# Optimization experiments

Measured on AMD Instinct MI355X. Metric: run time of the kernel, lower is better.

Reference implementation:

```python
import jax, jax.numpy as jnp
import numpy as np

B, D_IN, H, A, L, HEADS, C = 1024, 512, 768, 5001, 4, 2, 2
N_DATA = 56000.0
NEG = -1e30


def _gru_step(x, h, Wih, Whh, bih, bhh):
    # torch nn.GRU gate order: r, z, n
    gi = x @ Wih + bih            # [B, 3H]
    gh = h @ Whh + bhh            # [B, 3H]
    i_r, i_z, i_n = jnp.split(gi, 3, axis=-1)
    h_r, h_z, h_n = jnp.split(gh, 3, axis=-1)
    r = jax.nn.sigmoid(i_r + h_r)
    z = jax.nn.sigmoid(i_z + h_z)
    n = jnp.tanh(i_n + r * h_n)
    return (1.0 - z) * n + z * h


def _atom_selector(cls, mask, Wih, Whh, bih, bhh, hW, hb, ae_w, key):
    # cls: [B, H]; mask: [B, A] int32 (mutable copy); dropout in eval mode (identity)
    h = jnp.zeros_like(cls)
    cur_in = cls
    ae_const = jax.lax.stop_gradient(ae_w)
    probs = []
    max_index = None
    rows = jnp.arange(B)
    for j in range(L):
        h = _gru_step(cur_in, h, Wih, Whh, bih, bhh)
        logits = h @ hW + hb                      # [B, A]
        if j == 0:
            col0 = jnp.where(mask.sum(axis=-1) == 0, 1, mask[:, 0])
            mask = mask.at[:, 0].set(col0)
        else:
            mask = jnp.where((max_index == 0)[:, None], 0, mask)
            mask = mask.at[:, 0].set(1)
        masked = jnp.where(mask > 0, logits, NEG)
        u = jax.random.uniform(jax.random.fold_in(key, j), (B, A), minval=1e-9, maxval=1.0)
        g = -jnp.log(-jnp.log(u))
        y_soft = jax.nn.softmax(masked + g, axis=-1)  # tau = 1
        ind = jnp.argmax(y_soft, axis=-1)             # [B]
        y_hard = jax.nn.one_hot(ind, A, dtype=y_soft.dtype)
        prob = y_hard + y_soft - jax.lax.stop_gradient(y_soft)  # straight-through
        mask = mask.at[rows, ind].set(0)              # scatter-zero chosen atoms
        probs.append(prob)
        max_index = ind
        cur_in = cls + prob @ ae_const                # atom embedding feedback
    return jnp.stack(probs, axis=1)                   # [B, L, A]


def reference(x, x_mask, W1, b1, W2, b2, W3, b3, gru_Wih, gru_Whh, gru_bih, gru_bhh,
              head_W, head_b, ae_w, ce_Wmu, ce_bmu, ce_Wcov, ce_bcov, alpha):
    # linear_base MLP
    h = jax.nn.relu(x @ W1 + b1)
    h = jax.nn.relu(h @ W2 + b2)
    h = h @ W3 + b3                                   # cls embedding [B, H]
    key = jax.random.key(42)
    atom_probs, cps = [], []
    for i in range(HEADS):
        ap = _atom_selector(h, x_mask, gru_Wih[i], gru_Whh[i], gru_bih[i], gru_bhh[i],
                            head_W[i], head_b[i], ae_w, jax.random.fold_in(key, i))
        atom_probs.append(ap)
        # consequent estimator stand-in: mu [B,C], coverage [B]
        pooled = ap.mean(axis=1)                      # [B, A]
        mu = jax.nn.sigmoid(pooled @ ce_Wmu + ce_bmu)
        coverage = jax.nn.sigmoid(pooled @ ce_Wcov + ce_bcov)
        n = coverage * N_DATA
        sf = (alpha[0] / n)[:, None]                  # [B, 1] -> broadcast to [B, C]
        cp = (mu + sf) / (1.0 + 2.0 * sf)
        cps.append(cp)
    mat_cp = jnp.stack(cps, axis=1)                   # [B, HEADS, C]
    out = jnp.log(mat_cp.mean(axis=1))                # [B, C]
    return out, jnp.stack(atom_probs, axis=1), mat_cp


def setup_inputs() -> dict:
    key = jax.random.key(0)
    ks = jax.random.split(key, 16)
    s = 0.02
    nrm = lambda k, sh: jax.random.normal(k, sh, dtype=jnp.float32) * s
    return {
        'x': jax.random.normal(ks[0], (B, D_IN), dtype=jnp.float32),
        'x_mask': jax.random.randint(ks[1], (B, A), 0, 2, dtype=jnp.int32),
        'W1': nrm(ks[2], (D_IN, H)), 'b1': jnp.zeros((H,), jnp.float32),
        'W2': nrm(ks[3], (H, H)), 'b2': jnp.zeros((H,), jnp.float32),
        'W3': nrm(ks[4], (H, H)), 'b3': jnp.zeros((H,), jnp.float32),
        'gru_Wih': nrm(ks[5], (HEADS, H, 3 * H)), 'gru_Whh': nrm(ks[6], (HEADS, H, 3 * H)),
        'gru_bih': jnp.zeros((HEADS, 3 * H), jnp.float32), 'gru_bhh': jnp.zeros((HEADS, 3 * H), jnp.float32),
        'head_W': nrm(ks[7], (HEADS, H, A)), 'head_b': jnp.zeros((HEADS, A), jnp.float32),
        'ae_w': nrm(ks[8], (A, H)),
        'ce_Wmu': nrm(ks[9], (A, C)), 'ce_bmu': jnp.zeros((C,), jnp.float32),
        'ce_Wcov': nrm(ks[10], (A,)), 'ce_bcov': jnp.zeros((), jnp.float32),
        'alpha': jnp.ones((1,), jnp.float32),
    }
```

## Files before the change

kernel.cpp:

```cpp
#include <hip/hip_runtime.h>
#include <hip/hip_bf16.h>
#include <stdint.h>
#include <stddef.h>

#define B_DIM   1024
#define DIN     512
#define H_DIM   768
#define A_DIM   5001
#define NHEADS  2
#define NSTEPS  4
#define C_DIM   2
#define NEG_VAL -1e30f
#define BH      (B_DIM * H_DIM)

typedef unsigned short u16;
typedef __attribute__((ext_vector_type(8))) short v8s;
typedef __attribute__((ext_vector_type(4))) float v4f;

typedef const __attribute__((address_space(1))) uint32_t* gas_ptr;
typedef __attribute__((address_space(3))) uint32_t* las_ptr;

__device__ __forceinline__ void load_lds16(const void* g, void* l) {
  __builtin_amdgcn_global_load_lds((gas_ptr)g, (las_ptr)l, 16, 0, 0);
}

__host__ __device__ inline uint32_t rotl32(uint32_t x, int d) {
  return (x << d) | (x >> (32 - d));
}

__host__ __device__ inline void threefry2x32(uint32_t k0, uint32_t k1,
                                             uint32_t x0, uint32_t x1,
                                             uint32_t& o0, uint32_t& o1) {
  uint32_t ks2 = k0 ^ k1 ^ 0x1BD11BDAu;
  x0 += k0; x1 += k1;
#define TFR(d) { x0 += x1; x1 = rotl32(x1, (d)); x1 ^= x0; }
  TFR(13) TFR(15) TFR(26) TFR(6)  x0 += k1;  x1 += ks2 + 1u;
  TFR(17) TFR(29) TFR(16) TFR(24) x0 += ks2; x1 += k0 + 2u;
  TFR(13) TFR(15) TFR(26) TFR(6)  x0 += k0;  x1 += k1 + 3u;
  TFR(17) TFR(29) TFR(16) TFR(24) x0 += k1;  x1 += ks2 + 4u;
  TFR(13) TFR(15) TFR(26) TFR(6)  x0 += ks2; x1 += k0 + 5u;
#undef TFR
  o0 = x0; o1 = x1;
}

__device__ inline float gumbel_noise(uint32_t k0, uint32_t k1, uint32_t idx) {
  uint32_t o0, o1;
  threefry2x32(k0, k1, 0u, idx, o0, o1);
  uint32_t bits = o0 ^ o1;
  float f = __uint_as_float(0x3f800000u | (bits >> 9)) - 1.0f;
  float u = fmaxf(1e-9f, f * (1.0f - 1e-9f) + 1e-9f);
  return -logf(-logf(u));
}

__device__ inline float sigmoidf_(float x) { return 0.5f * tanhf(0.5f * x) + 0.5f; }

__device__ inline void split_bf16(float x, u16& hi, u16& lo) {
  __hip_bfloat16 h = __float2bfloat16(x);
  float hf = __bfloat162float(h);
  __hip_bfloat16 l = __float2bfloat16(x - hf);
  hi = *(const u16*)&h;
  lo = *(const u16*)&l;
}

__global__ __launch_bounds__(256) void split_kernel(
    const float* __restrict__ in, u16* __restrict__ hi, u16* __restrict__ lo, int n) {
  int idx = blockIdx.x * blockDim.x + threadIdx.x;
  if (idx >= n) return;
  u16 h, l;
  split_bf16(in[idx], h, l);
  hi[idx] = h; lo[idx] = l;
}

struct TS { const float* W; u16* hi; u16* lo; int K; int N; };
struct TS9 { TS t[9]; };

__global__ __launch_bounds__(256) void transpose_split_b(TS9 ts) {
  const TS p = ts.t[blockIdx.z];
  const int k0 = blockIdx.y * 32, n0 = blockIdx.x * 32;
  if (k0 >= p.K || n0 >= p.N) return;
  __shared__ float tile[32][33];
  const int tx = threadIdx.x & 31, ty = threadIdx.x >> 5;
#pragma unroll
  for (int r = ty; r < 32; r += 8) {
    int n = n0 + tx;
    tile[r][tx] = (n < p.N) ? p.W[(size_t)(k0 + r) * p.N + n] : 0.0f;
  }
  __syncthreads();
#pragma unroll
  for (int r = ty; r < 32; r += 8) {
    int n = n0 + r, k = k0 + tx;
    if (n < p.N) {
      u16 h, l;
      split_bf16(tile[tx][r], h, l);
      p.hi[(size_t)n * p.K + k] = h;
      p.lo[(size_t)n * p.K + k] = l;
    }
  }
}

struct GemmS {
  const u16* Ah[4]; const u16* Al[4];
  const u16* Bh[4]; const u16* Bl[4];
  const float* bias[4];
  float* C[4];
  u16* Ch[4]; u16* Cl[4];
  int N[4]; int nbx[4]; long long ldc[4]; int act[4]; int dup[4];
};

__global__ __launch_bounds__(256, 2) void gemm_mfma(GemmS gs, int K, int nby) {
  const int e = blockIdx.y;
  const int nwg = gridDim.x;
  const int chunk = nwg >> 3;
  const int lid = (blockIdx.x & 7) * chunk + (blockIdx.x >> 3);
  const int by = lid % nby;
  const int bx = lid / nby;
  if (bx >= gs.nbx[e]) return;
  const int bm = by * 128, bn = bx * 128;
  const int N = gs.N[e];

  __shared__ __align__(16) u16 lds[2][4][128 * 32];

  const int tid = threadIdx.x;
  const int wv = tid >> 6, ln = tid & 63;
  const int wr = wv >> 1, wc = wv & 1;
  const int lk = ln >> 4;
  const int lm = ln & 15;
  const int fswz = (lm >> 1) & 3;

  const int lrow = ln >> 2;
  const int slot = (ln & 3) ^ ((lrow >> 1) & 3);
  const u16* tsrc = (wv == 0) ? gs.Ah[e] : (wv == 1) ? gs.Al[e]
                  : (wv == 2) ? gs.Bh[e] : gs.Bl[e];
  const int isB = (wv >= 2);
  const int rowbase = isB ? bn : bm;

#define STAGE(B, K0)                                                  \
  {                                                                   \
    _Pragma("unroll")                                                 \
    for (int i = 0; i < 8; ++i) {                                     \
      int gr = rowbase + i * 16 + lrow;                               \
      if (isB && gr >= N) gr = N - 1;                                 \
      load_lds16(tsrc + (size_t)gr * K + (K0) + slot * 8,             \
                 (void*)&lds[B][wv][i * 512]);                        \
    }                                                                 \
  }

  v4f acc[4][4];
#pragma unroll
  for (int i = 0; i < 4; ++i)
#pragma unroll
    for (int j = 0; j < 4; ++j) acc[i][j] = (v4f){0.f, 0.f, 0.f, 0.f};

  STAGE(0, 0)
  int buf = 0;
  for (int k0 = 0; k0 < K; k0 += 32) {
    __syncthreads();
    if (k0 + 32 < K) STAGE(buf ^ 1, k0 + 32)

    const u16* LAh = lds[buf][0];
    const u16* LAl = lds[buf][1];
    const u16* LBh = lds[buf][2];
    const u16* LBl = lds[buf][3];
    v8s ah[4], al[4], bh[4], bl[4];
#pragma unroll
    for (int mi = 0; mi < 4; ++mi) {
      const int r = wr * 64 + mi * 16 + lm;
      const int off = r * 32 + ((lk ^ fswz) * 8);
      ah[mi] = *(const v8s*)&LAh[off];
      al[mi] = *(const v8s*)&LAl[off];
    }
#pragma unroll
    for (int ni = 0; ni < 4; ++ni) {
      const int r = wc * 64 + ni * 16 + lm;
      const int off = r * 32 + ((lk ^ fswz) * 8);
      bh[ni] = *(const v8s*)&LBh[off];
      bl[ni] = *(const v8s*)&LBl[off];
    }
#pragma unroll
    for (int mi = 0; mi < 4; ++mi)
#pragma unroll
      for (int ni = 0; ni < 4; ++ni)
        acc[mi][ni] = __builtin_amdgcn_mfma_f32_16x16x32_bf16(ah[mi], bh[ni], acc[mi][ni], 0, 0, 0);
#pragma unroll
    for (int mi = 0; mi < 4; ++mi)
#pragma unroll
      for (int ni = 0; ni < 4; ++ni)
        acc[mi][ni] = __builtin_amdgcn_mfma_f32_16x16x32_bf16(ah[mi], bl[ni], acc[mi][ni], 0, 0, 0);
#pragma unroll
    for (int mi = 0; mi < 4; ++mi)
#pragma unroll
      for (int ni = 0; ni < 4; ++ni)
        acc[mi][ni] = __builtin_amdgcn_mfma_f32_16x16x32_bf16(al[mi], bh[ni], acc[mi][ni], 0, 0, 0);

    buf ^= 1;
  }

  const float* bias = gs.bias[e];
  const long long ldc = gs.ldc[e];
  const int act = gs.act[e];
  float* Cf = gs.C[e];
  u16* ch = gs.Ch[e]; u16* cl = gs.Cl[e];
  const int dup = gs.dup[e];
#pragma unroll
  for (int mi = 0; mi < 4; ++mi) {
    const int m = bm + wr * 64 + mi * 16 + lk * 4;
#pragma unroll
    for (int ni = 0; ni < 4; ++ni) {
      const int n = bn + wc * 64 + ni * 16 + lm;
      if (n < N) {
        const float bv = bias[n];
#pragma unroll
        for (int r = 0; r < 4; ++r) {
          float v = acc[mi][ni][r] + bv;
          if (act) v = fmaxf(v, 0.0f);
          const size_t ix = (size_t)(m + r) * ldc + n;
          if (Cf) Cf[ix] = v;
          if (ch) {
            u16 hh, ll;
            split_bf16(v, hh, ll);
            ch[ix] = hh; cl[ix] = ll;
            if (dup) { ch[ix + (size_t)BH] = hh; cl[ix + (size_t)BH] = ll; }
          }
        }
      }
    }
  }
#undef STAGE
}

__global__ __launch_bounds__(256) void gru_combine_first(
    const float* __restrict__ gi2, const float* __restrict__ gbhh, float* __restrict__ h2,
    u16* __restrict__ h_hi, u16* __restrict__ h_lo) {
  int idx = blockIdx.x * blockDim.x + threadIdx.x;
  if (idx >= 2 * BH) return;
  int e = idx / BH, rem = idx % BH;
  int b = rem / H_DIM, c = rem - b * H_DIM;
  const float* gib = gi2 + ((size_t)e * B_DIM + b) * 3 * H_DIM;
  const float* bb = gbhh + (size_t)e * 3 * H_DIM;
  float ir = gib[c], iz = gib[H_DIM + c], inn = gib[2 * H_DIM + c];
  float hr = bb[c], hz = bb[H_DIM + c], hn = bb[2 * H_DIM + c];
  float r = sigmoidf_(ir + hr);
  float z = sigmoidf_(iz + hz);
  float n = tanhf(inn + r * hn);
  float hv = (1.0f - z) * n + z * 0.0f;
  h2[idx] = hv;
  u16 h, l;
  split_bf16(hv, h, l);
  h_hi[idx] = h; h_lo[idx] = l;
}

__global__ __launch_bounds__(256) void gru_combine_kernel(
    const float* __restrict__ gi2, const float* __restrict__ gh2, float* __restrict__ h2,
    u16* __restrict__ h_hi, u16* __restrict__ h_lo) {
  int idx = blockIdx.x * blockDim.x + threadIdx.x;
  if (idx >= 2 * BH) return;
  int e = idx / BH, rem = idx % BH;
  int b = rem / H_DIM, c = rem - b * H_DIM;
  const float* gib = gi2 + ((size_t)e * B_DIM + b) * 3 * H_DIM;
  const float* ghb = gh2 + ((size_t)e * B_DIM + b) * 3 * H_DIM;
  float ir = gib[c], iz = gib[H_DIM + c], inn = gib[2 * H_DIM + c];
  float hr = ghb[c], hz = ghb[H_DIM + c], hn = ghb[2 * H_DIM + c];
  float r = sigmoidf_(ir + hr);
  float z = sigmoidf_(iz + hz);
  float n = tanhf(inn + r * hn);
  float hv = (1.0f - z) * n + z * h2[idx];
  h2[idx] = hv;
  u16 h, l;
  split_bf16(hv, h, l);
  h_hi[idx] = h; h_lo[idx] = l;
}

#define STH 256
#define PER_TH 20

__global__ __launch_bounds__(STH) void sample_kernel(
    float* __restrict__ probs, const int* __restrict__ x_mask,
    int* __restrict__ indb, int j, uint4 keys,
    const float* __restrict__ cls, const float* __restrict__ ae_w,
    u16* __restrict__ cur_hi, u16* __restrict__ cur_lo, int docur) {
  int b = blockIdx.x;
  int e = blockIdx.y;
  int t = threadIdx.x;
  uint32_t k0 = (e == 0) ? keys.x : keys.z;
  uint32_t k1 = (e == 0) ? keys.y : keys.w;
  __shared__ float rv[STH];
  __shared__ int ri[STH];
  __shared__ int s_ind;

  float* prow = probs + (((size_t)b * NHEADS + e) * NSTEPS + j) * A_DIM;
  const int* mrow = x_mask + (size_t)b * A_DIM;

  int prev[3];
  bool dead = false;
  for (int tt = 0; tt < j; ++tt) {
    prev[tt] = indb[(e * NSTEPS + tt) * B_DIM + b];
    if (prev[tt] == 0) dead = true;
  }

  bool rowany = true;
  if (j == 0) {
    int any = 0;
    for (int a = t; a < A_DIM; a += STH) any |= mrow[a];
    ri[t] = any; __syncthreads();
    for (int s = STH / 2; s > 0; s >>= 1) {
      if (t < s) ri[t] |= ri[t + s];
      __syncthreads();
    }
    rowany = (ri[0] != 0);
    __syncthreads();
  }

  float v[PER_TH];
  float lmax = -3.0e38f;
#pragma unroll
  for (int s = 0; s < PER_TH; ++s) {
    int a = t + s * STH;
    float val = -3.0e38f;
    if (a < A_DIM) {
      int m;
      if (j == 0) {
        m = (a == 0) ? (rowany ? mrow[0] : 1) : mrow[a];
      } else if (a == 0) {
        m = 1;
      } else if (dead) {
        m = 0;
      } else {
        m = mrow[a];
        if (m) {
          for (int tt = 0; tt < j; ++tt)
            if (prev[tt] == a) { m = 0; break; }
        }
      }
      if (m > 0)
        val = prow[a] + gumbel_noise(k0, k1, (uint32_t)(b * A_DIM + a));
    }
    v[s] = val;
    lmax = fmaxf(lmax, val);
  }

  rv[t] = lmax; __syncthreads();
  for (int s = STH / 2; s > 0; s >>= 1) {
    if (t < s) rv[t] = fmaxf(rv[t], rv[t + s]);
    __syncthreads();
  }
  float m = rv[0]; __syncthreads();

  float lsum = 0.0f;
#pragma unroll
  for (int s = 0; s < PER_TH; ++s) {
    int a = t + s * STH;
    float ev = (a < A_DIM && v[s] > -1.0e37f) ? expf(v[s] - m) : 0.0f;
    v[s] = ev; lsum += ev;
  }
  rv[t] = lsum; __syncthreads();
  for (int s = STH / 2; s > 0; s >>= 1) {
    if (t < s) rv[t] += rv[t + s];
    __syncthreads();
  }
  float ssum = rv[0]; __syncthreads();

  float besty = -1.0f; int besti = A_DIM;
#pragma unroll
  for (int s = 0; s < PER_TH; ++s) {
    int a = t + s * STH;
    if (a < A_DIM) {
      float y = v[s] / ssum;
      if (y > besty) { besty = y; besti = a; }
    }
  }
  rv[t] = besty; ri[t] = besti; __syncthreads();
  for (int s = STH / 2; s > 0; s >>= 1) {
    if (t < s) {
      float y2 = rv[t + s]; int i2 = ri[t + s];
      if (y2 > rv[t] || (y2 == rv[t] && i2 < ri[t])) { rv[t] = y2; ri[t] = i2; }
    }
    __syncthreads();
  }
  if (t == 0) { s_ind = ri[0]; indb[(e * NSTEPS + j) * B_DIM + b] = ri[0]; }
  __syncthreads();
  int ind = s_ind;

  for (int a = t; a < A_DIM; a += STH) prow[a] = (a == ind) ? 1.0f : 0.0f;

  if (docur) {
    const float* crow = cls + (size_t)b * H_DIM;
    const float* arow = ae_w + (size_t)ind * H_DIM;
    u16* chh = cur_hi + (size_t)e * BH + (size_t)b * H_DIM;
    u16* cll = cur_lo + (size_t)e * BH + (size_t)b * H_DIM;
    for (int c = t; c < H_DIM; c += STH) {
      float vv = crow[c] + arow[c];
      u16 hh, ll;
      split_bf16(vv, hh, ll);
      chh[c] = hh; cll[c] = ll;
    }
  }
}

__global__ __launch_bounds__(256) void head_final_kernel(
    const int* __restrict__ indb, const float* __restrict__ Wmu,
    const float* __restrict__ bmu, const float* __restrict__ Wcov,
    const float* __restrict__ bcov, const float* __restrict__ alpha,
    float* __restrict__ matcp) {
  int idx = blockIdx.x * blockDim.x + threadIdx.x;
  if (idx >= NHEADS * B_DIM) return;
  int e = idx / B_DIM, b = idx - e * B_DIM;
  float a0 = 0.0f, a1 = 0.0f, ac = 0.0f;
  for (int j = 0; j < NSTEPS; ++j) {
    int ind = indb[(e * NSTEPS + j) * B_DIM + b];
    a0 += 0.25f * Wmu[(size_t)ind * C_DIM + 0];
    a1 += 0.25f * Wmu[(size_t)ind * C_DIM + 1];
    ac += 0.25f * Wcov[ind];
  }
  float mu0 = sigmoidf_(a0 + bmu[0]);
  float mu1 = sigmoidf_(a1 + bmu[1]);
  float cov = sigmoidf_(ac + bcov[0]);
  float n = cov * 56000.0f;
  float sf = alpha[0] / n;
  float denom = 1.0f + 2.0f * sf;
  matcp[((size_t)b * NHEADS + e) * C_DIM + 0] = (mu0 + sf) / denom;
  matcp[((size_t)b * NHEADS + e) * C_DIM + 1] = (mu1 + sf) / denom;
}

__global__ __launch_bounds__(256) void final_out_kernel(
    const float* __restrict__ matcp, float* __restrict__ out) {
  int idx = blockIdx.x * blockDim.x + threadIdx.x;
  if (idx >= B_DIM * C_DIM) return;
  int b = idx / C_DIM, c = idx - b * C_DIM;
  float s = matcp[((size_t)b * NHEADS + 0) * C_DIM + c] +
            matcp[((size_t)b * NHEADS + 1) * C_DIM + c];
  out[idx] = logf(s * 0.5f);
}

extern "C" void kernel_launch(void* const* d_in, const int* in_sizes, int n_in,
                              void* d_out, int out_size, void* d_ws, size_t ws_size,
                              hipStream_t stream) {
  const float* x     = (const float*)d_in[0];
  const int*   xmask = (const int*)d_in[1];
  const float* W1 = (const float*)d_in[2];  const float* b1 = (const float*)d_in[3];
  const float* W2 = (const float*)d_in[4];  const float* b2 = (const float*)d_in[5];
  const float* W3 = (const float*)d_in[6];  const float* b3 = (const float*)d_in[7];
  const float* gWih = (const float*)d_in[8];  const float* gWhh = (const float*)d_in[9];
  const float* gbih = (const float*)d_in[10]; const float* gbhh = (const float*)d_in[11];
  const float* hW = (const float*)d_in[12];   const float* hb = (const float*)d_in[13];
  const float* ae_w = (const float*)d_in[14];
  const float* Wmu  = (const float*)d_in[15]; const float* bmu  = (const float*)d_in[16];
  const float* Wcov = (const float*)d_in[17]; const float* bcov = (const float*)d_in[18];
  const float* alpha = (const float*)d_in[19];

  float* out = (float*)d_out;
  float* probs = out + (size_t)B_DIM * C_DIM;
  float* matcp = probs + (size_t)B_DIM * NHEADS * NSTEPS * A_DIM;

  const int HG = 3 * H_DIM;
  uint8_t* wsp = (uint8_t*)d_ws;
  auto alloc = [&](size_t bytes) {
    uint8_t* p = wsp;
    wsp += (bytes + 255) & ~(size_t)255;
    return p;
  };
  float* cls  = (float*)alloc((size_t)BH * 4);
  float* h2   = (float*)alloc((size_t)2 * BH * 4);
  float* gi2  = (float*)alloc((size_t)2 * B_DIM * HG * 4);
  float* gh2  = (float*)alloc((size_t)2 * B_DIM * HG * 4);
  u16* h_hi   = (u16*)alloc((size_t)2 * BH * 2);
  u16* h_lo   = (u16*)alloc((size_t)2 * BH * 2);
  u16* cur_hi = (u16*)alloc((size_t)2 * BH * 2);
  u16* cur_lo = (u16*)alloc((size_t)2 * BH * 2);
  u16* WihT_h = (u16*)alloc((size_t)2 * HG * H_DIM * 2);
  u16* WihT_l = (u16*)alloc((size_t)2 * HG * H_DIM * 2);
  u16* WhhT_h = (u16*)alloc((size_t)2 * HG * H_DIM * 2);
  u16* WhhT_l = (u16*)alloc((size_t)2 * HG * H_DIM * 2);
  u16* hWT_h  = (u16*)alloc((size_t)2 * A_DIM * H_DIM * 2);
  u16* hWT_l  = (u16*)alloc((size_t)2 * A_DIM * H_DIM * 2);
  u16* x_hi   = (u16*)alloc((size_t)B_DIM * DIN * 2);
  u16* x_lo   = (u16*)alloc((size_t)B_DIM * DIN * 2);
  u16* t1_hi  = (u16*)alloc((size_t)BH * 2);
  u16* t1_lo  = (u16*)alloc((size_t)BH * 2);
  u16* t2_hi  = (u16*)alloc((size_t)BH * 2);
  u16* t2_lo  = (u16*)alloc((size_t)BH * 2);
  u16* W1T_h  = (u16*)alloc((size_t)H_DIM * DIN * 2);
  u16* W1T_l  = (u16*)alloc((size_t)H_DIM * DIN * 2);
  u16* W2T_h  = (u16*)alloc((size_t)H_DIM * H_DIM * 2);
  u16* W2T_l  = (u16*)alloc((size_t)H_DIM * H_DIM * 2);
  u16* W3T_h  = (u16*)alloc((size_t)H_DIM * H_DIM * 2);
  u16* W3T_l  = (u16*)alloc((size_t)H_DIM * H_DIM * 2);
  int* indb   = (int*)alloc((size_t)NHEADS * NSTEPS * B_DIM * 4);

  dim3 blk(256);

  {
    TS9 ts;
    ts.t[0] = {gWih,                    WihT_h,                    WihT_l,                    H_DIM, HG};
    ts.t[1] = {gWih + (size_t)H_DIM*HG, WihT_h + (size_t)HG*H_DIM, WihT_l + (size_t)HG*H_DIM, H_DIM, HG};
    ts.t[2] = {gWhh,                    WhhT_h,                    WhhT_l,                    H_DIM, HG};
    ts.t[3] = {gWhh + (size_t)H_DIM*HG, WhhT_h + (size_t)HG*H_DIM, WhhT_l + (size_t)HG*H_DIM, H_DIM, HG};
    ts.t[4] = {hW,                          hWT_h,                           hWT_l,                           H_DIM, A_DIM};
    ts.t[5] = {hW + (size_t)H_DIM*A_DIM,    hWT_h + (size_t)A_DIM*H_DIM,     hWT_l + (size_t)A_DIM*H_DIM,     H_DIM, A_DIM};
    ts.t[6] = {W1, W1T_h, W1T_l, DIN,   H_DIM};
    ts.t[7] = {W2, W2T_h, W2T_l, H_DIM, H_DIM};
    ts.t[8] = {W3, W3T_h, W3T_l, H_DIM, H_DIM};
    transpose_split_b<<<dim3((A_DIM + 31) / 32, H_DIM / 32, 9), blk, 0, stream>>>(ts);
  }
  split_kernel<<<(B_DIM * DIN + 255) / 256, blk, 0, stream>>>(x, x_hi, x_lo, B_DIM * DIN);

  auto setE = [](GemmS& g, int e, const u16* ah, const u16* al, const u16* bhp, const u16* blp,
                 const float* bias, float* Cf, u16* chp, u16* clp,
                 int N, int nbx, long long ldc, int act, int dup) {
    g.Ah[e] = ah; g.Al[e] = al; g.Bh[e] = bhp; g.Bl[e] = blp;
    g.bias[e] = bias; g.C[e] = Cf; g.Ch[e] = chp; g.Cl[e] = clp;
    g.N[e] = N; g.nbx[e] = nbx; g.ldc[e] = ldc; g.act[e] = act; g.dup[e] = dup;
  };

  {
    GemmS g{};
    setE(g, 0, x_hi, x_lo, W1T_h, W1T_l, b1, nullptr, t1_hi, t1_lo, H_DIM, H_DIM / 128, H_DIM, 1, 0);
    gemm_mfma<<<dim3((H_DIM / 128) * 8, 1), blk, 0, stream>>>(g, DIN, 8);
  }
  {
    GemmS g{};
    setE(g, 0, t1_hi, t1_lo, W2T_h, W2T_l, b2, nullptr, t2_hi, t2_lo, H_DIM, H_DIM / 128, H_DIM, 1, 0);
    gemm_mfma<<<dim3((H_DIM / 128) * 8, 1), blk, 0, stream>>>(g, H_DIM, 8);
  }
  {
    GemmS g{};
    setE(g, 0, t2_hi, t2_lo, W3T_h, W3T_l, b3, cls, cur_hi, cur_lo, H_DIM, H_DIM / 128, H_DIM, 0, 1);
    gemm_mfma<<<dim3((H_DIM / 128) * 8, 1), blk, 0, stream>>>(g, H_DIM, 8);
  }

  uint32_t bk0 = 0u, bk1 = 42u;
  uint32_t hk[2][2];
  threefry2x32(bk0, bk1, 0u, 0u, hk[0][0], hk[0][1]);
  threefry2x32(bk0, bk1, 0u, 1u, hk[1][0], hk[1][1]);

  const int NBX_L = (A_DIM + 127) / 128;
  const int NBX_G = HG / 128;

  for (int j = 0; j < NSTEPS; ++j) {
    if (j == 0) {
      GemmS g{};
      for (int head = 0; head < NHEADS; ++head)
        setE(g, head, cur_hi + (size_t)head * BH, cur_lo + (size_t)head * BH,
             WihT_h + (size_t)head * HG * H_DIM, WihT_l + (size_t)head * HG * H_DIM,
             gbih + (size_t)head * HG, gi2 + (size_t)head * B_DIM * HG, nullptr, nullptr,
             HG, NBX_G, HG, 0, 0);
      gemm_mfma<<<dim3(NBX_G * 8, 2), blk, 0, stream>>>(g, H_DIM, 8);
      gru_combine_first<<<(2 * BH + 255) / 256, blk, 0, stream>>>(gi2, gbhh, h2, h_hi, h_lo);
    } else {
      GemmS g{};
      for (int head = 0; head < NHEADS; ++head) {
        setE(g, head * 2 + 0, cur_hi + (size_t)head * BH, cur_lo + (size_t)head * BH,
             WihT_h + (size_t)head * HG * H_DIM, WihT_l + (size_t)head * HG * H_DIM,
             gbih + (size_t)head * HG, gi2 + (size_t)head * B_DIM * HG, nullptr, nullptr,
             HG, NBX_G, HG, 0, 0);
        setE(g, head * 2 + 1, h_hi + (size_t)head * BH, h_lo + (size_t)head * BH,
             WhhT_h + (size_t)head * HG * H_DIM, WhhT_l + (size_t)head * HG * H_DIM,
             gbhh + (size_t)head * HG, gh2 + (size_t)head * B_DIM * HG, nullptr, nullptr,
             HG, NBX_G, HG, 0, 0);
      }
      gemm_mfma<<<dim3(NBX_G * 8, 4), blk, 0, stream>>>(g, H_DIM, 8);
      gru_combine_kernel<<<(2 * BH + 255) / 256, blk, 0, stream>>>(gi2, gh2, h2, h_hi, h_lo);
    }

    {
      GemmS g{};
      for (int head = 0; head < NHEADS; ++head)
        setE(g, head, h_hi + (size_t)head * BH, h_lo + (size_t)head * BH,
             hWT_h + (size_t)head * A_DIM * H_DIM, hWT_l + (size_t)head * A_DIM * H_DIM,
             hb + (size_t)head * A_DIM, probs + (size_t)(head * NSTEPS + j) * A_DIM,
             nullptr, nullptr, A_DIM, NBX_L, (long long)NHEADS * NSTEPS * A_DIM, 0, 0);
      gemm_mfma<<<dim3(NBX_L * 8, 2), blk, 0, stream>>>(g, H_DIM, 8);
    }

    uint32_t s00, s01, s10, s11;
    threefry2x32(hk[0][0], hk[0][1], 0u, (uint32_t)j, s00, s01);
    threefry2x32(hk[1][0], hk[1][1], 0u, (uint32_t)j, s10, s11);
    uint4 keys; keys.x = s00; keys.y = s01; keys.z = s10; keys.w = s11;
    sample_kernel<<<dim3(B_DIM, NHEADS), dim3(STH), 0, stream>>>(
        probs, xmask, indb, j, keys, cls, ae_w, cur_hi, cur_lo, (j < NSTEPS - 1) ? 1 : 0);
  }

  head_final_kernel<<<(NHEADS * B_DIM + 255) / 256, blk, 0, stream>>>(
      indb, Wmu, bmu, Wcov, bcov, alpha, matcp);
  final_out_kernel<<<(B_DIM * C_DIM + 255) / 256, blk, 0, stream>>>(matcp, out);
}
```

Baseline: 865.8 us.

## Shrink GEMM N-tile to 64, drop LDS double buffering, raise occupancy

The MFMA GEMM now uses 128x64 output tiles instead of 128x128, halving the B-operand LDS footprint and accumulator registers, and launch bounds rise to allow four blocks per CU. The double-buffered prefetch pipeline is replaced by a single-buffer load, sync, compute, sync loop. The aim is more concurrent waves and more blocks for the small-N GEMMs, at the cost of less reuse of A tiles and no overlap of global-to-LDS loads with compute within a block. HG becomes a macro, which is a cleanup.

```diff
diff --git a/kernel.cpp b/kernel.cpp
--- a/kernel.cpp
+++ b/kernel.cpp
@@ -12,6 +12,7 @@
 #define C_DIM   2
 #define NEG_VAL -1e30f
 #define BH      (B_DIM * H_DIM)
+#define HG      (3 * H_DIM)
 
 typedef unsigned short u16;
 typedef __attribute__((ext_vector_type(8))) short v8s;
@@ -107,7 +108,7 @@
   int N[4]; int nbx[4]; long long ldc[4]; int act[4]; int dup[4];
 };
 
-__global__ __launch_bounds__(256, 2) void gemm_mfma(GemmS gs, int K, int nby) {
+__global__ __launch_bounds__(256, 4) void gemm_mfma(GemmS gs, int K, int nby) {
   const int e = blockIdx.y;
   const int nwg = gridDim.x;
   const int chunk = nwg >> 3;
@@ -115,10 +116,11 @@
   const int by = lid % nby;
   const int bx = lid / nby;
   if (bx >= gs.nbx[e]) return;
-  const int bm = by * 128, bn = bx * 128;
+  const int bm = by * 128, bn = bx * 64;
   const int N = gs.N[e];
 
-  __shared__ __align__(16) u16 lds[2][4][128 * 32];
+  __shared__ __align__(16) u16 ldsA[2][128 * 32];
+  __shared__ __align__(16) u16 ldsB[2][64 * 32];
 
   const int tid = threadIdx.x;
   const int wv = tid >> 6, ln = tid & 63;
@@ -133,66 +135,56 @@
                   : (wv == 2) ? gs.Bh[e] : gs.Bl[e];
   const int isB = (wv >= 2);
   const int rowbase = isB ? bn : bm;
-
-#define STAGE(B, K0)                                                  \
-  {                                                                   \
-    _Pragma("unroll")                                                 \
-    for (int i = 0; i < 8; ++i) {                                     \
-      int gr = rowbase + i * 16 + lrow;                               \
-      if (isB && gr >= N) gr = N - 1;                                 \
-      load_lds16(tsrc + (size_t)gr * K + (K0) + slot * 8,             \
-                 (void*)&lds[B][wv][i * 512]);                        \
-    }                                                                 \
-  }
-
-  v4f acc[4][4];
+  u16* ldst = isB ? ldsB[wv - 2] : ldsA[wv];
+  const int nIss = isB ? 4 : 8;
+
+  v4f acc[4][2];
 #pragma unroll
   for (int i = 0; i < 4; ++i)
 #pragma unroll
-    for (int j = 0; j < 4; ++j) acc[i][j] = (v4f){0.f, 0.f, 0.f, 0.f};
-
-  STAGE(0, 0)
-  int buf = 0;
-  for (int k0 = 0; k0 < K; k0 += 32) {
+    for (int j = 0; j < 2; ++j) acc[i][j] = (v4f){0.f, 0.f, 0.f, 0.f};
+
+  for (int kt = 0; kt < K; kt += 32) {
+    for (int i = 0; i < nIss; ++i) {
+      int gr = rowbase + i * 16 + lrow;
+      if (isB && gr >= N) gr = N - 1;
+      const u16* gp = tsrc + (size_t)gr * K + kt + slot * 8;
+      load_lds16(gp, (void*)&ldst[i * 512]);
+    }
     __syncthreads();
-    if (k0 + 32 < K) STAGE(buf ^ 1, k0 + 32)
-
-    const u16* LAh = lds[buf][0];
-    const u16* LAl = lds[buf][1];
-    const u16* LBh = lds[buf][2];
-    const u16* LBl = lds[buf][3];
-    v8s ah[4], al[4], bh[4], bl[4];
+
+    v8s ah[4], al[4], bh[2], bl[2];
 #pragma unroll
     for (int mi = 0; mi < 4; ++mi) {
       const int r = wr * 64 + mi * 16 + lm;
       const int off = r * 32 + ((lk ^ fswz) * 8);
-      ah[mi] = *(const v8s*)&LAh[off];
-      al[mi] = *(const v8s*)&LAl[off];
-    }
-#pragma unroll
-    for (int ni = 0; ni < 4; ++ni) {
-      const int r = wc * 64 + ni * 16 + lm;
+      ah[mi] = *(const v8s*)&ldsA[0][off];
+      al[mi] = *(const v8s*)&ldsA[1][off];
+    }
+#pragma unroll
+    for (int ni = 0; ni < 2; ++ni) {
+      const int r = wc * 32 + ni * 16 + lm;
       const int off = r * 32 + ((lk ^ fswz) * 8);
-      bh[ni] = *(const v8s*)&LBh[off];
-      bl[ni] = *(const v8s*)&LBl[off];
+      bh[ni] = *(const v8s*)&ldsB[0][off];
+      bl[ni] = *(const v8s*)&ldsB[1][off];
     }
 #pragma unroll
     for (int mi = 0; mi < 4; ++mi)
 #pragma unroll
-      for (int ni = 0; ni < 4; ++ni)
+      for (int ni = 0; ni < 2; ++ni)
         acc[mi][ni] = __builtin_amdgcn_mfma_f32_16x16x32_bf16(ah[mi], bh[ni], acc[mi][ni], 0, 0, 0);
 #pragma unroll
     for (int mi = 0; mi < 4; ++mi)
 #pragma unroll
-      for (int ni = 0; ni < 4; ++ni)
+      for (int ni = 0; ni < 2; ++ni)
         acc[mi][ni] = __builtin_amdgcn_mfma_f32_16x16x32_bf16(ah[mi], bl[ni], acc[mi][ni], 0, 0, 0);
 #pragma unroll
     for (int mi = 0; mi < 4; ++mi)
 #pragma unroll
-      for (int ni = 0; ni < 4; ++ni)
+      for (int ni = 0; ni < 2; ++ni)
         acc[mi][ni] = __builtin_amdgcn_mfma_f32_16x16x32_bf16(al[mi], bh[ni], acc[mi][ni], 0, 0, 0);
 
-    buf ^= 1;
+    __syncthreads();
   }
 
   const float* bias = gs.bias[e];
@@ -205,8 +197,8 @@
   for (int mi = 0; mi < 4; ++mi) {
     const int m = bm + wr * 64 + mi * 16 + lk * 4;
 #pragma unroll
-    for (int ni = 0; ni < 4; ++ni) {
-      const int n = bn + wc * 64 + ni * 16 + lm;
+    for (int ni = 0; ni < 2; ++ni) {
+      const int n = bn + wc * 32 + ni * 16 + lm;
       if (n < N) {
         const float bv = bias[n];
 #pragma unroll
@@ -225,7 +217,6 @@
       }
     }
   }
-#undef STAGE
 }
 
 __global__ __launch_bounds__(256) void gru_combine_first(
@@ -235,8 +226,8 @@
   if (idx >= 2 * BH) return;
   int e = idx / BH, rem = idx % BH;
   int b = rem / H_DIM, c = rem - b * H_DIM;
-  const float* gib = gi2 + ((size_t)e * B_DIM + b) * 3 * H_DIM;
-  const float* bb = gbhh + (size_t)e * 3 * H_DIM;
+  const float* gib = gi2 + ((size_t)e * B_DIM + b) * HG;
+  const float* bb = gbhh + (size_t)e * HG;
   float ir = gib[c], iz = gib[H_DIM + c], inn = gib[2 * H_DIM + c];
   float hr = bb[c], hz = bb[H_DIM + c], hn = bb[2 * H_DIM + c];
   float r = sigmoidf_(ir + hr);
@@ -256,8 +247,8 @@
   if (idx >= 2 * BH) return;
   int e = idx / BH, rem = idx % BH;
   int b = rem / H_DIM, c = rem - b * H_DIM;
-  const float* gib = gi2 + ((size_t)e * B_DIM + b) * 3 * H_DIM;
-  const float* ghb = gh2 + ((size_t)e * B_DIM + b) * 3 * H_DIM;
+  const float* gib = gi2 + ((size_t)e * B_DIM + b) * HG;
+  const float* ghb = gh2 + ((size_t)e * B_DIM + b) * HG;
   float ir = gib[c], iz = gib[H_DIM + c], inn = gib[2 * H_DIM + c];
   float hr = ghb[c], hz = ghb[H_DIM + c], hn = ghb[2 * H_DIM + c];
   float r = sigmoidf_(ir + hr);
@@ -451,7 +442,6 @@
   float* probs = out + (size_t)B_DIM * C_DIM;
   float* matcp = probs + (size_t)B_DIM * NHEADS * NSTEPS * A_DIM;
 
-  const int HG = 3 * H_DIM;
   uint8_t* wsp = (uint8_t*)d_ws;
   auto alloc = [&](size_t bytes) {
     uint8_t* p = wsp;
@@ -511,29 +501,30 @@
     g.N[e] = N; g.nbx[e] = nbx; g.ldc[e] = ldc; g.act[e] = act; g.dup[e] = dup;
   };
 
+  const int NBX_M = H_DIM / 64;
+  const int NBX_G = HG / 64;
+  const int NBX_L = (A_DIM + 63) / 64;
+
   {
     GemmS g{};
-    setE(g, 0, x_hi, x_lo, W1T_h, W1T_l, b1, nullptr, t1_hi, t1_lo, H_DIM, H_DIM / 128, H_DIM, 1, 0);
-    gemm_mfma<<<dim3((H_DIM / 128) * 8, 1), blk, 0, stream>>>(g, DIN, 8);
+    setE(g, 0, x_hi, x_lo, W1T_h, W1T_l, b1, nullptr, t1_hi, t1_lo, H_DIM, NBX_M, H_DIM, 1, 0);
+    gemm_mfma<<<dim3(NBX_M * 8, 1), blk, 0, stream>>>(g, DIN, 8);
   }
   {
     GemmS g{};
-    setE(g, 0, t1_hi, t1_lo, W2T_h, W2T_l, b2, nullptr, t2_hi, t2_lo, H_DIM, H_DIM / 128, H_DIM, 1, 0);
-    gemm_mfma<<<dim3((H_DIM / 128) * 8, 1), blk, 0, stream>>>(g, H_DIM, 8);
+    setE(g, 0, t1_hi, t1_lo, W2T_h, W2T_l, b2, nullptr, t2_hi, t2_lo, H_DIM, NBX_M, H_DIM, 1, 0);
+    gemm_mfma<<<dim3(NBX_M * 8, 1), blk, 0, stream>>>(g, H_DIM, 8);
   }
   {
     GemmS g{};
-    setE(g, 0, t2_hi, t2_lo, W3T_h, W3T_l, b3, cls, cur_hi, cur_lo, H_DIM, H_DIM / 128, H_DIM, 0, 1);
-    gemm_mfma<<<dim3((H_DIM / 128) * 8, 1), blk, 0, stream>>>(g, H_DIM, 8);
+    setE(g, 0, t2_hi, t2_lo, W3T_h, W3T_l, b3, cls, cur_hi, cur_lo, H_DIM, NBX_M, H_DIM, 0, 1);
+    gemm_mfma<<<dim3(NBX_M * 8, 1), blk, 0, stream>>>(g, H_DIM, 8);
   }
 
   uint32_t bk0 = 0u, bk1 = 42u;
   uint32_t hk[2][2];
   threefry2x32(bk0, bk1, 0u, 0u, hk[0][0], hk[0][1]);
   threefry2x32(bk0, bk1, 0u, 1u, hk[1][0], hk[1][1]);
-
-  const int NBX_L = (A_DIM + 127) / 128;
-  const int NBX_G = HG / 128;
 
   for (int j = 0; j < NSTEPS; ++j) {
     if (j == 0) {
```

Result: no change. 864.0 us (-0.2%).
